# Performance work log

Hardware: AMD Instinct MI355X
Metric: run time of the kernel (lower is better)

Reference implementation:

```python
import jax, jax.numpy as jnp
import numpy as np

PART_INDICES = [[0, 1, 2, 3, 4], [5, 6, 11, 12], [5, 7, 9], [6, 8, 10], [11, 12, 13, 14, 15, 16]]
B, J, D_IN, D_H, D_OUT = 4096, 25, 512, 256, 512


def _xavier(key, shape):
    fan_in, fan_out = shape
    lim = float(np.sqrt(6.0 / (fan_in + fan_out)))
    return jax.random.uniform(key, shape, jnp.float32, -lim, lim)


def setup_inputs() -> dict:
    key = jax.random.key(0)
    ks = list(jax.random.split(key, 64))
    it = iter(ks)
    inp = {}
    inp["x"] = jax.random.normal(next(it), (B, J, D_IN), jnp.float32)
    inp["adj_global"] = jax.random.uniform(next(it), (J, J), jnp.float32)
    for p, idx in enumerate(PART_INDICES):
        n = len(idx)
        inp[f"adj_local_{p}"] = jax.random.uniform(next(it), (n, n), jnp.float32)
    # global GCN params (2 layers)
    inp["Wg0"] = _xavier(next(it), (D_IN, D_H)); inp["bg0"] = jnp.zeros((D_H,), jnp.float32)
    inp["Wg1"] = _xavier(next(it), (D_H, D_OUT)); inp["bg1"] = jnp.zeros((D_OUT,), jnp.float32)
    # local GCN params (5 parts x 2 layers)
    for p in range(5):
        inp[f"Wl{p}a"] = _xavier(next(it), (D_IN, D_H)); inp[f"bl{p}a"] = jnp.zeros((D_H,), jnp.float32)
        inp[f"Wl{p}b"] = _xavier(next(it), (D_H, D_OUT)); inp[f"bl{p}b"] = jnp.zeros((D_OUT,), jnp.float32)
    # fusion MLP: Linear(2*D_OUT, D_OUT) -> ReLU -> Linear(D_OUT, D_OUT)
    inp["Wf0"] = _xavier(next(it), (2 * D_OUT, D_OUT)); inp["bf0"] = jnp.zeros((D_OUT,), jnp.float32)
    inp["Wf1"] = _xavier(next(it), (D_OUT, D_OUT)); inp["bf1"] = jnp.zeros((D_OUT,), jnp.float32)
    return inp


def _gcn(x, adj, W, b):
    # symmetric degree normalization D^-1/2 A D^-1/2, then (norm_adj @ (x @ W)) + b
    d = jnp.clip(adj.sum(axis=1), 1e-6, None) ** -0.5
    norm_adj = d[:, None] * adj * d[None, :]                       # [n, n]
    return jnp.einsum('ij,bjf->bif', norm_adj, x @ W) + b          # [B, n, out]


def reference(x, adj_global, adj_local_0, adj_local_1, adj_local_2, adj_local_3, adj_local_4,
              Wg0, bg0, Wg1, bg1,
              Wl0a, bl0a, Wl0b, bl0b,
              Wl1a, bl1a, Wl1b, bl1b,
              Wl2a, bl2a, Wl2b, bl2b,
              Wl3a, bl3a, Wl3b, bl3b,
              Wl4a, bl4a, Wl4b, bl4b,
              Wf0, bf0, Wf1, bf1):
    adjs = [adj_local_0, adj_local_1, adj_local_2, adj_local_3, adj_local_4]
    lps = [(Wl0a, bl0a, Wl0b, bl0b), (Wl1a, bl1a, Wl1b, bl1b), (Wl2a, bl2a, Wl2b, bl2b),
           (Wl3a, bl3a, Wl3b, bl3b), (Wl4a, bl4a, Wl4b, bl4b)]
    # global branch
    xg = jax.nn.relu(_gcn(x, adj_global, Wg0, bg0))
    xg = jax.nn.relu(_gcn(xg, adj_global, Wg1, bg1))
    # local branch: scatter per-part outputs back (later parts overwrite overlaps, like torch)
    xl = jnp.zeros((x.shape[0], x.shape[1], D_OUT), x.dtype)
    for p, idx in enumerate(PART_INDICES):
        Wa, ba, Wb, bb = lps[p]
        idx_a = jnp.asarray(idx)
        xp = x[:, idx_a]                                           # [B, n_p, D_IN]
        xp = jax.nn.relu(_gcn(xp, adjs[p], Wa, ba))
        xp = jax.nn.relu(_gcn(xp, adjs[p], Wb, bb))
        xl = xl.at[:, idx_a].set(xp)
    # fusion MLP
    xc = jnp.concatenate([xg, xl], axis=-1)                        # [B, J, 2*D_OUT]
    return jax.nn.relu(xc @ Wf0 + bf0) @ Wf1 + bf1                 # [B, J, D_OUT]
```

## Files before the change

### kernel.cpp

```cpp
#include <hip/hip_runtime.h>


#define BATCH 4096
#define NJOINT 25
#define MROWS (BATCH * NJOINT)
#define SZ_FULL (MROWS * 512)

typedef __attribute__((ext_vector_type(8))) short short8;
typedef __attribute__((ext_vector_type(4))) float float4_;

__device__ __forceinline__ float b2f(ushort u) {
    union { float f; uint32_t i; } x; x.i = ((uint32_t)u) << 16; return x.f;
}
__device__ __forceinline__ ushort f2b(float f) {
    union { float f; uint32_t i; } x; x.f = f;
    uint32_t r = x.i + 0x7fff + ((x.i >> 16) & 1);
    return (ushort)(r >> 16);
}
__device__ __forceinline__ void async16(const void* g, void* l) {
    __builtin_amdgcn_global_load_lds(
        (const __attribute__((address_space(1))) void*)g,
        (__attribute__((address_space(3))) void*)l, 16, 0, 0);
}

__device__ void norm_one(const float* A, int n, float* out, float* sAdj, float* sD) {
    int t = threadIdx.x;
    for (int i = t; i < n * n; i += 256) sAdj[i] = A[i];
    __syncthreads();
    if (t < n) {
        float s = 0.f;
        for (int j = 0; j < n; j++) s += sAdj[t * n + j];
        sD[t] = 1.0f / sqrtf(fmaxf(s, 1e-6f));
    }
    __syncthreads();
    for (int i = t; i < n * n; i += 256) {
        int r = i / n, c = i % n;
        out[i] = sD[r] * sAdj[i] * sD[c];
    }
    __syncthreads();
}

__global__ __launch_bounds__(256) void adjnorm_kernel(
    const float* Ag, const float* A0, const float* A2, const float* A3,
    const float* A4, float* ADJ) {
    __shared__ float sAdj[640];
    __shared__ float sD[32];
    norm_one(Ag, 25, ADJ, sAdj, sD);
    norm_one(A0, 5, ADJ + 640 + 0 * 64, sAdj, sD);
    norm_one(A2, 3, ADJ + 640 + 1 * 64, sAdj, sD);
    norm_one(A3, 3, ADJ + 640 + 2 * 64, sAdj, sD);
    norm_one(A4, 6, ADJ + 640 + 3 * 64, sAdj, sD);
}

__global__ __launch_bounds__(256) void cvt_bf16(const float* __restrict__ in,
                                                ushort* __restrict__ out, int n4) {
    int id = blockIdx.x * 256 + threadIdx.x;
    if (id < n4) {
        float4 v = ((const float4*)in)[id];
        ushort4 o;
        o.x = f2b(v.x); o.y = f2b(v.y); o.z = f2b(v.z); o.w = f2b(v.w);
        ((ushort4*)out)[id] = o;
    }
}

__global__ __launch_bounds__(256) void wtrans(const float* __restrict__ W,
                                              ushort* __restrict__ Wt, int K, int N) {
    __shared__ float tile[32][33];
    int t = threadIdx.x;
    int tx = t & 31, ty = t >> 5;
    int k0 = blockIdx.y * 32, n0 = blockIdx.x * 32;
    for (int r = ty; r < 32; r += 8)
        tile[r][tx] = W[(size_t)(k0 + r) * N + n0 + tx];
    __syncthreads();
    for (int r = ty; r < 32; r += 8)
        Wt[(size_t)(n0 + r) * K + k0 + tx] = f2b(tile[tx][r]);
}

__global__ __launch_bounds__(256) void zero_tail(ushort* __restrict__ XGL) {
    int id = blockIdx.x * 256 + threadIdx.x;
    int f4 = id & 127;
    int rj = (id >> 7) & 7;
    int b = id >> 10;
    ushort4 z; z.x = 0; z.y = 0; z.z = 0; z.w = 0;
    ((ushort4*)(XGL + ((size_t)(b * 25 + 17 + rj) * 1024 + 512)))[f4] = z;
}

template <bool GATHER, bool BIAS, bool RELU, bool OUTF32>
__global__ __launch_bounds__(512, 2) void gemm256(
    const ushort* __restrict__ A, const ushort* __restrict__ Wt,
    const float* __restrict__ bias, void* __restrict__ C,
    int M, int N, int K, int lda, int ldc,
    int gn, int g0, int g1, int g2, int g3, int g4, int g5) {
    __shared__ ushort lds[65536];
    int t = threadIdx.x;
    int l = t & 63, w = t >> 6;

    int nwg = (int)gridDim.x;
    int cpx = nwg >> 3;
    int wg = ((int)blockIdx.x & 7) * cpx + ((int)blockIdx.x >> 3);
    int gx = N >> 8;
    int tm = wg / gx, tn = wg - tm * gx;
    int bm = tm << 8, bn = tn << 8;

    int srow = (w << 4) + (l >> 3);
    int sch = ((l & 7) ^ (l >> 3)) << 3;
    const ushort* pA[2][2];
    const ushort* pB[2][2];
    {
        int map_[6] = {g0, g1, g2, g3, g4, g5};
#pragma unroll
        for (int h = 0; h < 2; h++)
#pragma unroll
            for (int i = 0; i < 2; i++) {
                int r = bm + h * 128 + srow + i * 8;
                if (GATHER) { int b = r / gn; r = b * 25 + map_[r - b * gn]; }
                pA[h][i] = A + (size_t)r * lda + sch;
                int c = bn + h * 128 + srow + i * 8;
                pB[h][i] = Wt + (size_t)c * K + sch;
            }
    }
    int stga = w << 10;

    int wm = w >> 2, wn = w & 3;
    int lr = l & 15, q = l >> 4;
    int cx = lr & 7;
    int ca0 = (q ^ cx) << 3;
    int ca1 = ca0 ^ 32;
    int ra = (wm << 13) + (lr << 6);
    int rb = 16384 + ((wn >> 1) << 13) + ((wn & 1) << 12) + (lr << 6);

    float4_ acc[8][4];
#pragma unroll
    for (int fi = 0; fi < 8; fi++)
#pragma unroll
        for (int fj = 0; fj < 4; fj++) acc[fi][fj] = (float4_)0.f;
    short8 bfr[4][2];

#define STG_A(DB, H, KT) do {                                              \
        async16(pA[H][0] + (KT) * 64, &lds[(DB) + (H) * 8192 + stga]);     \
        async16(pA[H][1] + (KT) * 64, &lds[(DB) + (H) * 8192 + stga + 512]); \
    } while (0)
#define STG_B(DB, H, KT) do {                                              \
        async16(pB[H][0] + (KT) * 64, &lds[(DB) + 16384 + (H) * 8192 + stga]); \
        async16(pB[H][1] + (KT) * 64, &lds[(DB) + 16384 + (H) * 8192 + stga + 512]); \
    } while (0)

#define DO_PHASE(DB, FI0, RDB, WAITST, ...) do {                           \
        short8 af00, af01, af10, af11;                                     \
        if (RDB) {                                                         \
            _Pragma("unroll")                                              \
            for (int fj = 0; fj < 4; fj++) {                               \
                bfr[fj][0] = *(const short8*)&lds[(DB) + rb + fj * 1024 + ca0]; \
                bfr[fj][1] = *(const short8*)&lds[(DB) + rb + fj * 1024 + ca1]; \
            }                                                              \
        }                                                                  \
        af00 = *(const short8*)&lds[(DB) + ra + (FI0) * 1024 + ca0];       \
        af01 = *(const short8*)&lds[(DB) + ra + (FI0) * 1024 + ca1];       \
        af10 = *(const short8*)&lds[(DB) + ra + ((FI0) + 1) * 1024 + ca0]; \
        af11 = *(const short8*)&lds[(DB) + ra + ((FI0) + 1) * 1024 + ca1]; \
        __VA_ARGS__                                                        \
        WAITST                                                             \
        if (RDB) asm volatile("s_waitcnt lgkmcnt(8)");                     \
        __builtin_amdgcn_sched_barrier(0);                                 \
        __builtin_amdgcn_s_barrier();                                      \
        asm volatile("s_waitcnt lgkmcnt(0)" ::: "memory");                 \
        __builtin_amdgcn_sched_barrier(0);                                 \
        __builtin_amdgcn_s_setprio(1);                                     \
        _Pragma("unroll")                                                  \
        for (int fj = 0; fj < 4; fj++) {                                   \
            acc[FI0][fj] = __builtin_amdgcn_mfma_f32_16x16x32_bf16(        \
                af00, bfr[fj][0], acc[FI0][fj], 0, 0, 0);                  \
            acc[FI0][fj] = __builtin_amdgcn_mfma_f32_16x16x32_bf16(        \
                af01, bfr[fj][1], acc[FI0][fj], 0, 0, 0);                  \
            acc[(FI0) + 1][fj] = __builtin_amdgcn_mfma_f32_16x16x32_bf16(  \
                af10, bfr[fj][0], acc[(FI0) + 1][fj], 0, 0, 0);            \
            acc[(FI0) + 1][fj] = __builtin_amdgcn_mfma_f32_16x16x32_bf16(  \
                af11, bfr[fj][1], acc[(FI0) + 1][fj], 0, 0, 0);            \
        }                                                                  \
        __builtin_amdgcn_s_setprio(0);                                     \
        __builtin_amdgcn_sched_barrier(0);                                 \
        __builtin_amdgcn_s_barrier();                                      \
    } while (0)

    int NT = K >> 6;
    int NITER = NT >> 1;

    STG_A(0, 0, 0); STG_A(0, 1, 0);
    STG_B(0, 0, 0); STG_B(0, 1, 0);
    STG_B(32768, 0, 1); STG_B(32768, 1, 1);
    asm volatile("s_waitcnt vmcnt(4)" ::: "memory");
    __builtin_amdgcn_sched_barrier(0);
    __builtin_amdgcn_s_barrier();

    for (int j = 0; j < NITER; ++j) {
        int k1 = 2 * j + 1, k2 = 2 * j + 2, k3 = 2 * j + 3;
        bool nl = (j + 1 < NITER);
        DO_PHASE(0, 0, true, , STG_A(32768, 0, k1););
        DO_PHASE(0, 2, false, , STG_A(32768, 1, k1););
        DO_PHASE(0, 4, false, , if (nl) STG_B(0, 0, k2););
        DO_PHASE(0, 6, false,
                 if (nl) { asm volatile("s_waitcnt vmcnt(4)" ::: "memory"); }
                 else    { asm volatile("s_waitcnt vmcnt(0)" ::: "memory"); },
                 if (nl) STG_B(0, 1, k2););
        DO_PHASE(32768, 0, true, , if (nl) STG_A(0, 0, k2););
        DO_PHASE(32768, 2, false, , if (nl) STG_A(0, 1, k2););
        DO_PHASE(32768, 4, false, , if (nl) STG_B(32768, 0, k3););
        DO_PHASE(32768, 6, false,
                 if (nl) { asm volatile("s_waitcnt vmcnt(4)" ::: "memory"); },
                 if (nl) STG_B(32768, 1, k3););
    }
#undef DO_PHASE
#undef STG_A
#undef STG_B

    int cl = lr;
    float bv[4];
#pragma unroll
    for (int fj = 0; fj < 4; fj++)
        bv[fj] = BIAS ? bias[bn + (wn << 6) + (fj << 4) + cl] : 0.f;
#pragma unroll
    for (int fi = 0; fi < 8; fi++) {
        int row0 = bm + (wm << 7) + (fi << 4) + (q << 2);
#pragma unroll
        for (int r = 0; r < 4; r++) {
            size_t rowoff = (size_t)(row0 + r) * ldc;
#pragma unroll
            for (int fj = 0; fj < 4; fj++) {
                int col = bn + (wn << 6) + (fj << 4) + cl;
                float v = acc[fi][fj][r] + bv[fj];
                if (RELU) v = fmaxf(v, 0.f);
                if (OUTF32)
                    ((float*)C)[rowoff + col] = v;
                else
                    ((ushort*)C)[rowoff + col] = f2b(v);
            }
        }
    }
    (void)M;
}

template <int NJ>
__global__ __launch_bounds__(256) void mix_inplace(
    ushort* __restrict__ T, const float* __restrict__ adjn,
    const float* __restrict__ bias, int F, int ldr) {
    __shared__ float As[NJ * NJ];
    int t = threadIdx.x;
    for (int i = t; i < NJ * NJ; i += 256) As[i] = adjn[i];
    __syncthreads();
    int id = blockIdx.x * 256 + t;
    int f = id % F;
    int b = id / F;
    ushort* base = T + (size_t)(b * NJ) * ldr + f;
    float v[NJ];
#pragma unroll
    for (int j = 0; j < NJ; j++) v[j] = b2f(base[(size_t)j * ldr]);
    float bi = bias[f];
#pragma unroll
    for (int i = 0; i < NJ; i++) {
        float o = 0.f;
#pragma unroll
        for (int j = 0; j < NJ; j++) o += As[i * NJ + j] * v[j];
        base[(size_t)i * ldr] = f2b(fmaxf(o + bi, 0.f));
    }
}

template <int NJ>
__global__ __launch_bounds__(256) void mix_scatter(
    const ushort* __restrict__ P, const float* __restrict__ adjn,
    const float* __restrict__ bias, ushort* __restrict__ XL,
    int j0, int j1, int j2, int j3, int j4, int j5) {
    __shared__ float As[NJ * NJ];
    __shared__ int jm[NJ];
    int t = threadIdx.x;
    for (int i = t; i < NJ * NJ; i += 256) As[i] = adjn[i];
    if (t == 0) {
        int tmp[6] = {j0, j1, j2, j3, j4, j5};
        for (int i = 0; i < NJ; i++) jm[i] = tmp[i];
    }
    __syncthreads();
    int id = blockIdx.x * 256 + t;
    int f = id & 511;
    int b = id >> 9;
    float v[NJ];
    const ushort* base = P + (size_t)(b * NJ) * 512 + f;
#pragma unroll
    for (int j = 0; j < NJ; j++) v[j] = b2f(base[(size_t)j * 512]);
    float bi = bias[f];
#pragma unroll
    for (int i = 0; i < NJ; i++) {
        float o = 0.f;
#pragma unroll
        for (int j = 0; j < NJ; j++) o += As[i * NJ + j] * v[j];
        XL[((size_t)(b * 25 + jm[i])) * 1024 + f] = f2b(fmaxf(o + bi, 0.f));
    }
}

extern "C" void kernel_launch(void* const* d_in, const int* in_sizes, int n_in,
                              void* d_out, int out_size, void* d_ws,
                              size_t ws_size, hipStream_t stream) {
    const float* x    = (const float*)d_in[0];
    const float* adjg = (const float*)d_in[1];
    const float* al0  = (const float*)d_in[2];
    const float* al2  = (const float*)d_in[4];
    const float* al3  = (const float*)d_in[5];
    const float* al4  = (const float*)d_in[6];
    const float* Wg0  = (const float*)d_in[7];
    const float* bg0  = (const float*)d_in[8];
    const float* Wg1  = (const float*)d_in[9];
    const float* bg1  = (const float*)d_in[10];
    const float* Wf0  = (const float*)d_in[31];
    const float* bf0  = (const float*)d_in[32];
    const float* Wf1  = (const float*)d_in[33];
    const float* bf1  = (const float*)d_in[34];

    float* ws = (float*)d_ws;
    float* ADJ = ws;
    ushort* U  = (ushort*)(ws + 4096);
    ushort* Xb  = U;
    ushort* XGL = U + (size_t)SZ_FULL;
    ushort* S   = XGL + (size_t)MROWS * 1024;
    ushort* T  = S;
    ushort* P1 = S;
    ushort* P3 = S + 6291456;
    ushort* Wb = S + 26214400;
    ushort* HF = Xb;

    ushort* Wg0t = Wb;
    ushort* Wg1t = Wb + 131072;
    ushort* Wf0t = Wb + 1310720;
    ushort* Wf1t = Wb + 1835008;

    dim3 blk(256);
    dim3 blk512(512);

    adjnorm_kernel<<<1, blk, 0, stream>>>(adjg, al0, al2, al3, al4, ADJ);
    cvt_bf16<<<SZ_FULL / 4 / 256, blk, 0, stream>>>(x, Xb, SZ_FULL / 4);
    zero_tail<<<16384, blk, 0, stream>>>(XGL);

    wtrans<<<dim3(256 / 32, 512 / 32), blk, 0, stream>>>(Wg0, Wg0t, 512, 256);
    wtrans<<<dim3(512 / 32, 256 / 32), blk, 0, stream>>>(Wg1, Wg1t, 256, 512);
    wtrans<<<dim3(512 / 32, 1024 / 32), blk, 0, stream>>>(Wf0, Wf0t, 1024, 512);
    wtrans<<<dim3(512 / 32, 512 / 32), blk, 0, stream>>>(Wf1, Wf1t, 512, 512);

    struct Part { int n, widx; int idx[6]; };
    const Part parts[4] = {
        {5, 11, {0, 1, 2, 3, 4, 0}},
        {3, 19, {5, 7, 9, 0, 0, 0}},
        {3, 23, {6, 8, 10, 0, 0, 0}},
        {6, 27, {11, 12, 13, 14, 15, 16}},
    };
    for (int q = 0; q < 4; q++) {
        ushort* Wat = Wb + 262144 + q * 262144;
        ushort* Wbt = Wat + 131072;
        wtrans<<<dim3(8, 16), blk, 0, stream>>>((const float*)d_in[parts[q].widx], Wat, 512, 256);
        wtrans<<<dim3(16, 8), blk, 0, stream>>>((const float*)d_in[parts[q].widx + 2], Wbt, 256, 512);
    }

    gemm256<false, false, false, false><<<400, blk512, 0, stream>>>(
        Xb, Wg0t, nullptr, T, MROWS, 256, 512, 512, 256, 0, 0, 0, 0, 0, 0, 0);
    mix_inplace<25><<<BATCH * 256 / 256, blk, 0, stream>>>(T, ADJ, bg0, 256, 256);
    gemm256<false, false, false, false><<<800, blk512, 0, stream>>>(
        T, Wg1t, nullptr, XGL, MROWS, 512, 256, 256, 1024, 0, 0, 0, 0, 0, 0, 0);
    mix_inplace<25><<<BATCH * 512 / 256, blk, 0, stream>>>(XGL, ADJ, bg1, 512, 1024);

    const int slots[4] = {0, 1, 2, 3};
    for (int q = 0; q < 4; q++) {
        const Part& P = parts[q];
        const float* ba = (const float*)d_in[P.widx + 1];
        const float* bb = (const float*)d_in[P.widx + 3];
        ushort* Wat = Wb + 262144 + q * 262144;
        ushort* Wbt = Wat + 131072;
        const float* adjl = ADJ + 640 + slots[q] * 64;
        int M = BATCH * P.n;
        gemm256<true, false, false, false><<<M / 256, blk512, 0, stream>>>(
            Xb, Wat, nullptr, P1, M, 256, 512, 512, 256,
            P.n, P.idx[0], P.idx[1], P.idx[2], P.idx[3], P.idx[4], P.idx[5]);
        if (P.n == 5)
            mix_inplace<5><<<BATCH * 256 / 256, blk, 0, stream>>>(P1, adjl, ba, 256, 256);
        else if (P.n == 3)
            mix_inplace<3><<<BATCH * 256 / 256, blk, 0, stream>>>(P1, adjl, ba, 256, 256);
        else
            mix_inplace<6><<<BATCH * 256 / 256, blk, 0, stream>>>(P1, adjl, ba, 256, 256);
        gemm256<false, false, false, false><<<(M / 256) * 2, blk512, 0, stream>>>(
            P1, Wbt, nullptr, P3, M, 512, 256, 256, 512, 0, 0, 0, 0, 0, 0, 0);
        if (P.n == 5)
            mix_scatter<5><<<BATCH * 512 / 256, blk, 0, stream>>>(
                P3, adjl, bb, XGL + 512, P.idx[0], P.idx[1], P.idx[2], P.idx[3], P.idx[4], P.idx[5]);
        else if (P.n == 3)
            mix_scatter<3><<<BATCH * 512 / 256, blk, 0, stream>>>(
                P3, adjl, bb, XGL + 512, P.idx[0], P.idx[1], P.idx[2], P.idx[3], P.idx[4], P.idx[5]);
        else
            mix_scatter<6><<<BATCH * 512 / 256, blk, 0, stream>>>(
                P3, adjl, bb, XGL + 512, P.idx[0], P.idx[1], P.idx[2], P.idx[3], P.idx[4], P.idx[5]);
    }

    gemm256<false, true, true, false><<<800, blk512, 0, stream>>>(
        XGL, Wf0t, bf0, HF, MROWS, 512, 1024, 1024, 512, 0, 0, 0, 0, 0, 0, 0);
    gemm256<false, true, false, true><<<800, blk512, 0, stream>>>(
        HF, Wf1t, bf1, (float*)d_out, MROWS, 512, 512, 512, 512, 0, 0, 0, 0, 0, 0, 0);

    (void)in_sizes; (void)n_in; (void)out_size; (void)ws_size;
}
```

Baseline: 1.031 ms.

## Batch global and per-part GEMMs and mixes into grouped launches

Replaces the many small per-part launches with grouped kernels driven by descriptor tables. Weight transposes become one launch, the first- and second-layer GEMMs of the global and all local branches each become one launch, and the mix kernels become two grouped launches. The intent is to cut launch overhead and the tail underutilization of small per-part grids (e.g. 48-96 workgroups). Flags are now runtime values instead of template parameters, the explicit sched_barrier/lgkmcnt waits in the GEMM pipeline are dropped, and workspace buffers are re-laid out so the parts do not alias.

```diff
diff --git a/kernel.cpp b/kernel.cpp
--- a/kernel.cpp
+++ b/kernel.cpp
@@ -63,17 +63,26 @@
     }
 }
 
-__global__ __launch_bounds__(256) void wtrans(const float* __restrict__ W,
-                                              ushort* __restrict__ Wt, int K, int N) {
+struct WDesc { const float* W; ushort* Wt; int K, N, nxlog, end; };
+struct WParams { WDesc d[12]; };
+
+__global__ __launch_bounds__(256) void wtrans_all(WParams P) {
     __shared__ float tile[32][33];
-    int t = threadIdx.x;
-    int tx = t & 31, ty = t >> 5;
-    int k0 = blockIdx.y * 32, n0 = blockIdx.x * 32;
+    int bid = blockIdx.x;
+    int i = 0, start = 0;
+    while (bid >= P.d[i].end) { start = P.d[i].end; i++; }
+    const WDesc& D = P.d[i];
+    int local = bid - start;
+    int bx = local & ((1 << D.nxlog) - 1);
+    int by = local >> D.nxlog;
+    int K = D.K, N = D.N;
+    int t = threadIdx.x, tx = t & 31, ty = t >> 5;
+    int k0 = by * 32, n0 = bx * 32;
     for (int r = ty; r < 32; r += 8)
-        tile[r][tx] = W[(size_t)(k0 + r) * N + n0 + tx];
+        tile[r][tx] = D.W[(size_t)(k0 + r) * N + n0 + tx];
     __syncthreads();
     for (int r = ty; r < 32; r += 8)
-        Wt[(size_t)(n0 + r) * K + k0 + tx] = f2b(tile[tx][r]);
+        D.Wt[(size_t)(n0 + r) * K + k0 + tx] = f2b(tile[tx][r]);
 }
 
 __global__ __launch_bounds__(256) void zero_tail(ushort* __restrict__ XGL) {
@@ -85,12 +94,14 @@
     ((ushort4*)(XGL + ((size_t)(b * 25 + 17 + rj) * 1024 + 512)))[f4] = z;
 }
 
-template <bool GATHER, bool BIAS, bool RELU, bool OUTF32>
-__global__ __launch_bounds__(512, 2) void gemm256(
-    const ushort* __restrict__ A, const ushort* __restrict__ Wt,
-    const float* __restrict__ bias, void* __restrict__ C,
-    int M, int N, int K, int lda, int ldc,
-    int gn, int g0, int g1, int g2, int g3, int g4, int g5) {
+struct GDesc {
+    const ushort* A; const ushort* Wt; const float* bias; void* C;
+    int K, lda, ldc, nTiles, wgEnd, gn, flags, pad;
+    int gmap[6];
+};
+struct GParams { GDesc g[5]; };
+
+__global__ __launch_bounds__(512, 2) void gemmg(GParams P) {
     __shared__ ushort lds[65536];
     int t = threadIdx.x;
     int l = t & 63, w = t >> 6;
@@ -98,27 +109,35 @@
     int nwg = (int)gridDim.x;
     int cpx = nwg >> 3;
     int wg = ((int)blockIdx.x & 7) * cpx + ((int)blockIdx.x >> 3);
-    int gx = N >> 8;
-    int tm = wg / gx, tn = wg - tm * gx;
+
+    int gi = 0, wg0 = 0;
+    while (wg >= P.g[gi].wgEnd) { wg0 = P.g[gi].wgEnd; gi++; }
+    const GDesc& G = P.g[gi];
+    int lw = wg - wg0;
+    int tm, tn;
+    if (G.nTiles == 2) { tm = lw >> 1; tn = lw & 1; }
+    else               { tm = lw;      tn = 0; }
     int bm = tm << 8, bn = tn << 8;
+    const int K = G.K, lda = G.lda, ldc = G.ldc;
+    const bool GATHER = (G.flags & 1) != 0;
+    const bool BIAS   = (G.flags & 2) != 0;
+    const bool RELU   = (G.flags & 4) != 0;
+    const bool OUTF32 = (G.flags & 8) != 0;
 
     int srow = (w << 4) + (l >> 3);
     int sch = ((l & 7) ^ (l >> 3)) << 3;
     const ushort* pA[2][2];
     const ushort* pB[2][2];
-    {
-        int map_[6] = {g0, g1, g2, g3, g4, g5};
-#pragma unroll
-        for (int h = 0; h < 2; h++)
-#pragma unroll
-            for (int i = 0; i < 2; i++) {
-                int r = bm + h * 128 + srow + i * 8;
-                if (GATHER) { int b = r / gn; r = b * 25 + map_[r - b * gn]; }
-                pA[h][i] = A + (size_t)r * lda + sch;
-                int c = bn + h * 128 + srow + i * 8;
-                pB[h][i] = Wt + (size_t)c * K + sch;
-            }
-    }
+#pragma unroll
+    for (int h = 0; h < 2; h++)
+#pragma unroll
+        for (int i = 0; i < 2; i++) {
+            int r = bm + h * 128 + srow + i * 8;
+            if (GATHER) { int b = r / G.gn; r = b * 25 + G.gmap[r - b * G.gn]; }
+            pA[h][i] = G.A + (size_t)r * lda + sch;
+            int c = bn + h * 128 + srow + i * 8;
+            pB[h][i] = G.Wt + (size_t)c * K + sch;
+        }
     int stga = w << 10;
 
     int wm = w >> 2, wn = w & 3;
@@ -136,6 +155,7 @@
         for (int fj = 0; fj < 4; fj++) acc[fi][fj] = (float4_)0.f;
     short8 bfr[4][2];
 
+#define FENCE() asm volatile("" ::: "memory")
 #define STG_A(DB, H, KT) do {                                              \
         async16(pA[H][0] + (KT) * 64, &lds[(DB) + (H) * 8192 + stga]);     \
         async16(pA[H][1] + (KT) * 64, &lds[(DB) + (H) * 8192 + stga + 512]); \
@@ -145,7 +165,7 @@
         async16(pB[H][1] + (KT) * 64, &lds[(DB) + 16384 + (H) * 8192 + stga + 512]); \
     } while (0)
 
-#define DO_PHASE(DB, FI0, RDB, WAITST, ...) do {                           \
+#define DO_PHASE(DB, FI0, RDB, WAITST, STMT) do {                          \
         short8 af00, af01, af10, af11;                                     \
         if (RDB) {                                                         \
             _Pragma("unroll")                                              \
@@ -158,13 +178,10 @@
         af01 = *(const short8*)&lds[(DB) + ra + (FI0) * 1024 + ca1];       \
         af10 = *(const short8*)&lds[(DB) + ra + ((FI0) + 1) * 1024 + ca0]; \
         af11 = *(const short8*)&lds[(DB) + ra + ((FI0) + 1) * 1024 + ca1]; \
-        __VA_ARGS__                                                        \
+        STMT                                                               \
         WAITST                                                             \
-        if (RDB) asm volatile("s_waitcnt lgkmcnt(8)");                     \
-        __builtin_amdgcn_sched_barrier(0);                                 \
         __builtin_amdgcn_s_barrier();                                      \
-        asm volatile("s_waitcnt lgkmcnt(0)" ::: "memory");                 \
-        __builtin_amdgcn_sched_barrier(0);                                 \
+        FENCE();                                                           \
         __builtin_amdgcn_s_setprio(1);                                     \
         _Pragma("unroll")                                                  \
         for (int fj = 0; fj < 4; fj++) {                                   \
@@ -178,8 +195,8 @@
                 af11, bfr[fj][1], acc[(FI0) + 1][fj], 0, 0, 0);            \
         }                                                                  \
         __builtin_amdgcn_s_setprio(0);                                     \
-        __builtin_amdgcn_sched_barrier(0);                                 \
         __builtin_amdgcn_s_barrier();                                      \
+        FENCE();                                                           \
     } while (0)
 
     int NT = K >> 6;
@@ -189,8 +206,8 @@
     STG_B(0, 0, 0); STG_B(0, 1, 0);
     STG_B(32768, 0, 1); STG_B(32768, 1, 1);
     asm volatile("s_waitcnt vmcnt(4)" ::: "memory");
-    __builtin_amdgcn_sched_barrier(0);
     __builtin_amdgcn_s_barrier();
+    FENCE();
 
     for (int j = 0; j < NITER; ++j) {
         int k1 = 2 * j + 1, k2 = 2 * j + 2, k3 = 2 * j + 3;
@@ -212,12 +229,13 @@
 #undef DO_PHASE
 #undef STG_A
 #undef STG_B
+#undef FENCE
 
     int cl = lr;
     float bv[4];
 #pragma unroll
     for (int fj = 0; fj < 4; fj++)
-        bv[fj] = BIAS ? bias[bn + (wn << 6) + (fj << 4) + cl] : 0.f;
+        bv[fj] = BIAS ? G.bias[bn + (wn << 6) + (fj << 4) + cl] : 0.f;
 #pragma unroll
     for (int fi = 0; fi < 8; fi++) {
         int row0 = bm + (wm << 7) + (fi << 4) + (q << 2);
@@ -230,68 +248,92 @@
                 float v = acc[fi][fj][r] + bv[fj];
                 if (RELU) v = fmaxf(v, 0.f);
                 if (OUTF32)
-                    ((float*)C)[rowoff + col] = v;
+                    ((float*)G.C)[rowoff + col] = v;
                 else
-                    ((ushort*)C)[rowoff + col] = f2b(v);
+                    ((ushort*)G.C)[rowoff + col] = f2b(v);
             }
         }
     }
-    (void)M;
-}
+}
+
+struct M1Desc { ushort* T; const float* adj; const float* bias; int nj; };
+struct M1Params { M1Desc d[5]; };
 
 template <int NJ>
-__global__ __launch_bounds__(256) void mix_inplace(
-    ushort* __restrict__ T, const float* __restrict__ adjn,
-    const float* __restrict__ bias, int F, int ldr) {
-    __shared__ float As[NJ * NJ];
-    int t = threadIdx.x;
-    for (int i = t; i < NJ * NJ; i += 256) As[i] = adjn[i];
-    __syncthreads();
-    int id = blockIdx.x * 256 + t;
-    int f = id % F;
-    int b = id / F;
-    ushort* base = T + (size_t)(b * NJ) * ldr + f;
+__device__ __forceinline__ void mix1_body(ushort* base, const float* As, float bi) {
     float v[NJ];
 #pragma unroll
-    for (int j = 0; j < NJ; j++) v[j] = b2f(base[(size_t)j * ldr]);
-    float bi = bias[f];
+    for (int j = 0; j < NJ; j++) v[j] = b2f(base[(size_t)j * 256]);
 #pragma unroll
     for (int i = 0; i < NJ; i++) {
         float o = 0.f;
 #pragma unroll
         for (int j = 0; j < NJ; j++) o += As[i * NJ + j] * v[j];
-        base[(size_t)i * ldr] = f2b(fmaxf(o + bi, 0.f));
-    }
-}
+        base[(size_t)i * 256] = f2b(fmaxf(o + bi, 0.f));
+    }
+}
+
+__global__ __launch_bounds__(256) void mixg1(M1Params P) {
+    __shared__ float As[625];
+    int r = blockIdx.x >> 12;
+    const M1Desc& D = P.d[r];
+    int t = threadIdx.x;
+    int nj = D.nj;
+    for (int i = t; i < nj * nj; i += 256) As[i] = D.adj[i];
+    __syncthreads();
+    int id = ((blockIdx.x & 4095) << 8) + t;
+    int f = id & 255, b = id >> 8;
+    ushort* base = D.T + ((size_t)b * nj) * 256 + f;
+    float bi = D.bias[f];
+    switch (nj) {
+        case 25: mix1_body<25>(base, As, bi); break;
+        case 5:  mix1_body<5>(base, As, bi); break;
+        case 3:  mix1_body<3>(base, As, bi); break;
+        default: mix1_body<6>(base, As, bi); break;
+    }
+}
+
+struct M2Desc {
+    const ushort* src; ushort* dst; const float* adj; const float* bias;
+    int nj, sldr; int jm[25];
+};
+struct M2Params { M2Desc d[5]; };
 
 template <int NJ>
-__global__ __launch_bounds__(256) void mix_scatter(
-    const ushort* __restrict__ P, const float* __restrict__ adjn,
-    const float* __restrict__ bias, ushort* __restrict__ XL,
-    int j0, int j1, int j2, int j3, int j4, int j5) {
-    __shared__ float As[NJ * NJ];
-    __shared__ int jm[NJ];
-    int t = threadIdx.x;
-    for (int i = t; i < NJ * NJ; i += 256) As[i] = adjn[i];
-    if (t == 0) {
-        int tmp[6] = {j0, j1, j2, j3, j4, j5};
-        for (int i = 0; i < NJ; i++) jm[i] = tmp[i];
-    }
-    __syncthreads();
-    int id = blockIdx.x * 256 + t;
-    int f = id & 511;
-    int b = id >> 9;
+__device__ __forceinline__ void mix2_body(const ushort* src, int sldr, ushort* dst,
+                                          const int* jms, const float* As, float bi) {
     float v[NJ];
-    const ushort* base = P + (size_t)(b * NJ) * 512 + f;
-#pragma unroll
-    for (int j = 0; j < NJ; j++) v[j] = b2f(base[(size_t)j * 512]);
-    float bi = bias[f];
+#pragma unroll
+    for (int j = 0; j < NJ; j++) v[j] = b2f(src[(size_t)j * sldr]);
 #pragma unroll
     for (int i = 0; i < NJ; i++) {
         float o = 0.f;
 #pragma unroll
         for (int j = 0; j < NJ; j++) o += As[i * NJ + j] * v[j];
-        XL[((size_t)(b * 25 + jm[i])) * 1024 + f] = f2b(fmaxf(o + bi, 0.f));
+        dst[(size_t)jms[i] * 1024] = f2b(fmaxf(o + bi, 0.f));
+    }
+}
+
+__global__ __launch_bounds__(256) void mixg2(M2Params P) {
+    __shared__ float As[625];
+    __shared__ int jms[25];
+    int r = blockIdx.x >> 13;
+    const M2Desc& D = P.d[r];
+    int t = threadIdx.x;
+    int nj = D.nj;
+    for (int i = t; i < nj * nj; i += 256) As[i] = D.adj[i];
+    if (t < nj) jms[t] = D.jm[t];
+    __syncthreads();
+    int id = ((blockIdx.x & 8191) << 8) + t;
+    int f = id & 511, b = id >> 9;
+    const ushort* src = D.src + ((size_t)b * nj) * D.sldr + f;
+    ushort* dst = D.dst + (size_t)b * 25 * 1024 + f;
+    float bi = D.bias[f];
+    switch (nj) {
+        case 25: mix2_body<25>(src, D.sldr, dst, jms, As, bi); break;
+        case 5:  mix2_body<5>(src, D.sldr, dst, jms, As, bi); break;
+        case 3:  mix2_body<3>(src, D.sldr, dst, jms, As, bi); break;
+        default: mix2_body<6>(src, D.sldr, dst, jms, As, bi); break;
     }
 }
 
@@ -315,32 +357,20 @@
 
     float* ws = (float*)d_ws;
     float* ADJ = ws;
-    ushort* U  = (ushort*)(ws + 4096);
+    ushort* U   = (ushort*)(ws + 4096);
     ushort* Xb  = U;
-    ushort* XGL = U + (size_t)SZ_FULL;
-    ushort* S   = XGL + (size_t)MROWS * 1024;
-    ushort* T  = S;
-    ushort* P1 = S;
-    ushort* P3 = S + 6291456;
-    ushort* Wb = S + 26214400;
-    ushort* HF = Xb;
+    ushort* XGL = Xb + (size_t)SZ_FULL;
+    ushort* T   = XGL + (size_t)MROWS * 1024;
+    ushort* P1  = T + (size_t)MROWS * 256;
+    ushort* Wb  = P1 + (size_t)BATCH * 17 * 256;
+    ushort* P3  = Xb;
+    ushort* HF  = Xb;
 
     ushort* Wg0t = Wb;
     ushort* Wg1t = Wb + 131072;
-    ushort* Wf0t = Wb + 1310720;
-    ushort* Wf1t = Wb + 1835008;
-
-    dim3 blk(256);
-    dim3 blk512(512);
-
-    adjnorm_kernel<<<1, blk, 0, stream>>>(adjg, al0, al2, al3, al4, ADJ);
-    cvt_bf16<<<SZ_FULL / 4 / 256, blk, 0, stream>>>(x, Xb, SZ_FULL / 4);
-    zero_tail<<<16384, blk, 0, stream>>>(XGL);
-
-    wtrans<<<dim3(256 / 32, 512 / 32), blk, 0, stream>>>(Wg0, Wg0t, 512, 256);
-    wtrans<<<dim3(512 / 32, 256 / 32), blk, 0, stream>>>(Wg1, Wg1t, 256, 512);
-    wtrans<<<dim3(512 / 32, 1024 / 32), blk, 0, stream>>>(Wf0, Wf0t, 1024, 512);
-    wtrans<<<dim3(512 / 32, 512 / 32), blk, 0, stream>>>(Wf1, Wf1t, 512, 512);
+    ushort* Wf0t = Wb + 262144;
+    ushort* Wf1t = Wb + 786432;
+    ushort* Wpt  = Wb + 1048576;
 
     struct Part { int n, widx; int idx[6]; };
     const Part parts[4] = {
@@ -349,55 +379,108 @@
         {3, 23, {6, 8, 10, 0, 0, 0}},
         {6, 27, {11, 12, 13, 14, 15, 16}},
     };
-    for (int q = 0; q < 4; q++) {
-        ushort* Wat = Wb + 262144 + q * 262144;
-        ushort* Wbt = Wat + 131072;
-        wtrans<<<dim3(8, 16), blk, 0, stream>>>((const float*)d_in[parts[q].widx], Wat, 512, 256);
-        wtrans<<<dim3(16, 8), blk, 0, stream>>>((const float*)d_in[parts[q].widx + 2], Wbt, 256, 512);
-    }
-
-    gemm256<false, false, false, false><<<400, blk512, 0, stream>>>(
-        Xb, Wg0t, nullptr, T, MROWS, 256, 512, 512, 256, 0, 0, 0, 0, 0, 0, 0);
-    mix_inplace<25><<<BATCH * 256 / 256, blk, 0, stream>>>(T, ADJ, bg0, 256, 256);
-    gemm256<false, false, false, false><<<800, blk512, 0, stream>>>(
-        T, Wg1t, nullptr, XGL, MROWS, 512, 256, 256, 1024, 0, 0, 0, 0, 0, 0, 0);
-    mix_inplace<25><<<BATCH * 512 / 256, blk, 0, stream>>>(XGL, ADJ, bg1, 512, 1024);
-
-    const int slots[4] = {0, 1, 2, 3};
-    for (int q = 0; q < 4; q++) {
-        const Part& P = parts[q];
-        const float* ba = (const float*)d_in[P.widx + 1];
-        const float* bb = (const float*)d_in[P.widx + 3];
-        ushort* Wat = Wb + 262144 + q * 262144;
-        ushort* Wbt = Wat + 131072;
-        const float* adjl = ADJ + 640 + slots[q] * 64;
-        int M = BATCH * P.n;
-        gemm256<true, false, false, false><<<M / 256, blk512, 0, stream>>>(
-            Xb, Wat, nullptr, P1, M, 256, 512, 512, 256,
-            P.n, P.idx[0], P.idx[1], P.idx[2], P.idx[3], P.idx[4], P.idx[5]);
-        if (P.n == 5)
-            mix_inplace<5><<<BATCH * 256 / 256, blk, 0, stream>>>(P1, adjl, ba, 256, 256);
-        else if (P.n == 3)
-            mix_inplace<3><<<BATCH * 256 / 256, blk, 0, stream>>>(P1, adjl, ba, 256, 256);
-        else
-            mix_inplace<6><<<BATCH * 256 / 256, blk, 0, stream>>>(P1, adjl, ba, 256, 256);
-        gemm256<false, false, false, false><<<(M / 256) * 2, blk512, 0, stream>>>(
-            P1, Wbt, nullptr, P3, M, 512, 256, 256, 512, 0, 0, 0, 0, 0, 0, 0);
-        if (P.n == 5)
-            mix_scatter<5><<<BATCH * 512 / 256, blk, 0, stream>>>(
-                P3, adjl, bb, XGL + 512, P.idx[0], P.idx[1], P.idx[2], P.idx[3], P.idx[4], P.idx[5]);
-        else if (P.n == 3)
-            mix_scatter<3><<<BATCH * 512 / 256, blk, 0, stream>>>(
-                P3, adjl, bb, XGL + 512, P.idx[0], P.idx[1], P.idx[2], P.idx[3], P.idx[4], P.idx[5]);
-        else
-            mix_scatter<6><<<BATCH * 512 / 256, blk, 0, stream>>>(
-                P3, adjl, bb, XGL + 512, P.idx[0], P.idx[1], P.idx[2], P.idx[3], P.idx[4], P.idx[5]);
-    }
-
-    gemm256<false, true, true, false><<<800, blk512, 0, stream>>>(
-        XGL, Wf0t, bf0, HF, MROWS, 512, 1024, 1024, 512, 0, 0, 0, 0, 0, 0, 0);
-    gemm256<false, true, false, true><<<800, blk512, 0, stream>>>(
-        HF, Wf1t, bf1, (float*)d_out, MROWS, 512, 512, 512, 512, 0, 0, 0, 0, 0, 0, 0);
+    const int cumn[4] = {0, 5, 8, 11};
+
+    dim3 blk(256), blk512(512);
+
+    adjnorm_kernel<<<1, blk, 0, stream>>>(adjg, al0, al2, al3, al4, ADJ);
+    cvt_bf16<<<SZ_FULL / 4 / 256, blk, 0, stream>>>(x, Xb, SZ_FULL / 4);
+    zero_tail<<<16384, blk, 0, stream>>>(XGL);
+
+    {
+        WParams WP{};
+        int e = 0, i = 0;
+        auto add = [&](const float* W, ushort* Wt, int K, int N) {
+            int nx = N >> 5;
+            int nxlog = (nx == 8) ? 3 : ((nx == 16) ? 4 : 5);
+            e += nx * (K >> 5);
+            WP.d[i++] = {W, Wt, K, N, nxlog, e};
+        };
+        add(Wg0, Wg0t, 512, 256);
+        add(Wg1, Wg1t, 256, 512);
+        add(Wf0, Wf0t, 1024, 512);
+        add(Wf1, Wf1t, 512, 512);
+        for (int qv = 0; qv < 4; qv++) {
+            add((const float*)d_in[parts[qv].widx], Wpt + qv * 262144, 512, 256);
+            add((const float*)d_in[parts[qv].widx + 2], Wpt + qv * 262144 + 131072, 256, 512);
+        }
+        wtrans_all<<<2048, blk, 0, stream>>>(WP);
+    }
+
+    auto setg = [](GDesc& g, const ushort* A, const ushort* Wt, const float* bias,
+                   void* C, int K, int lda, int ldc, int nT, int wgEnd, int gn,
+                   int flags, const int* map) {
+        g.A = A; g.Wt = Wt; g.bias = bias; g.C = C; g.K = K; g.lda = lda;
+        g.ldc = ldc; g.nTiles = nT; g.wgEnd = wgEnd; g.gn = gn; g.flags = flags;
+        g.pad = 0;
+        for (int i = 0; i < 6; i++) g.gmap[i] = map ? map[i] : 0;
+    };
+
+    {
+        GParams GA{};
+        int e = 400;
+        setg(GA.g[0], Xb, Wg0t, nullptr, T, 512, 512, 256, 1, e, 0, 0, nullptr);
+        for (int qv = 0; qv < 4; qv++) {
+            e += parts[qv].n * 16;
+            setg(GA.g[1 + qv], Xb, Wpt + qv * 262144, nullptr,
+                 P1 + (size_t)BATCH * cumn[qv] * 256,
+                 512, 512, 256, 1, e, parts[qv].n, 1, parts[qv].idx);
+        }
+        gemmg<<<672, blk512, 0, stream>>>(GA);
+    }
+
+    {
+        M1Params M1{};
+        M1.d[0] = {T, ADJ, bg0, 25};
+        for (int qv = 0; qv < 4; qv++)
+            M1.d[1 + qv] = {P1 + (size_t)BATCH * cumn[qv] * 256,
+                            ADJ + 640 + qv * 64,
+                            (const float*)d_in[parts[qv].widx + 1],
+                            parts[qv].n};
+        mixg1<<<20480, blk, 0, stream>>>(M1);
+    }
+
+    {
+        GParams GB{};
+        int e = 800;
+        setg(GB.g[0], T, Wg1t, nullptr, XGL, 256, 256, 1024, 2, e, 0, 0, nullptr);
+        for (int qv = 0; qv < 4; qv++) {
+            e += parts[qv].n * 32;
+            setg(GB.g[1 + qv], P1 + (size_t)BATCH * cumn[qv] * 256,
+                 Wpt + qv * 262144 + 131072, nullptr,
+                 P3 + (size_t)BATCH * cumn[qv] * 512,
+                 256, 256, 512, 2, e, 0, 0, nullptr);
+        }
+        gemmg<<<1344, blk512, 0, stream>>>(GB);
+    }
+
+    {
+        M2Params M2{};
+        M2.d[0].src = XGL; M2.d[0].dst = XGL; M2.d[0].adj = ADJ;
+        M2.d[0].bias = bg1; M2.d[0].nj = 25; M2.d[0].sldr = 1024;
+        for (int i = 0; i < 25; i++) M2.d[0].jm[i] = i;
+        for (int qv = 0; qv < 4; qv++) {
+            M2Desc& D = M2.d[1 + qv];
+            D.src = P3 + (size_t)BATCH * cumn[qv] * 512;
+            D.dst = XGL + 512;
+            D.adj = ADJ + 640 + qv * 64;
+            D.bias = (const float*)d_in[parts[qv].widx + 3];
+            D.nj = parts[qv].n; D.sldr = 512;
+            for (int i = 0; i < 25; i++) D.jm[i] = (i < 6) ? parts[qv].idx[i] : 0;
+        }
+        mixg2<<<40960, blk, 0, stream>>>(M2);
+    }
+
+    {
+        GParams GF{};
+        setg(GF.g[0], XGL, Wf0t, bf0, HF, 1024, 1024, 512, 2, 800, 0, 2 | 4, nullptr);
+        gemmg<<<800, blk512, 0, stream>>>(GF);
+    }
+    {
+        GParams GO{};
+        setg(GO.g[0], HF, Wf1t, bf1, d_out, 512, 512, 512, 2, 800, 0, 2 | 8, nullptr);
+        gemmg<<<800, blk512, 0, stream>>>(GO);
+    }
 
     (void)in_sizes; (void)n_in; (void)out_size; (void)ws_size;
 }
```

Result: faster. 963.9 us (-6.5%).
